# Optimization experiments

Measured on AMD Instinct MI355X. Metric: run time of the kernel, lower is better.

## Reference

```python
import jax, jax.numpy as jnp
import numpy as np

H = 1024      # hidden_size
V = 32000     # output_size (vocab)
L = 128       # max_length (encoder length)
B = 256       # batch


def setup_inputs() -> dict:
    key = jax.random.key(0)
    ks = jax.random.split(key, 16)
    s = 1.0 / np.sqrt(H)
    inp = {
        "input_ids": jax.random.randint(ks[0], (1, B), 0, V),
        "hidden": jax.random.normal(ks[1], (1, B, H), dtype=jnp.float32),
        "encoder_outputs": jax.random.normal(ks[2], (B, L, H), dtype=jnp.float32),
        # parameters
        "emb_table": jax.random.normal(ks[3], (V, H), dtype=jnp.float32),
        "attn_w": jax.random.uniform(ks[4], (L, 2 * H), jnp.float32, -s, s),
        "attn_b": jax.random.uniform(ks[5], (L,), jnp.float32, -s, s),
        "comb_w": jax.random.uniform(ks[6], (H, 2 * H), jnp.float32, -s, s),
        "comb_b": jax.random.uniform(ks[7], (H,), jnp.float32, -s, s),
        "w_ih": jax.random.uniform(ks[8], (3 * H, H), jnp.float32, -s, s),
        "b_ih": jax.random.uniform(ks[9], (3 * H,), jnp.float32, -s, s),
        "w_hh": jax.random.uniform(ks[10], (3 * H, H), jnp.float32, -s, s),
        "b_hh": jax.random.uniform(ks[11], (3 * H,), jnp.float32, -s, s),
        "out_w": jax.random.uniform(ks[12], (V, H), jnp.float32, -s, s),
        "out_b": jax.random.uniform(ks[13], (V,), jnp.float32, -s, s),
    }
    return inp


def reference(input_ids, hidden, encoder_outputs, emb_table,
              attn_w, attn_b, comb_w, comb_b,
              w_ih, b_ih, w_hh, b_hh, out_w, out_b):
    # embedding: input_ids (1, B) -> embedded (1, B, H); dropout is identity in eval
    embedded = emb_table[input_ids]            # (1, B, H)
    emb0 = embedded[0]                         # (B, H)
    h0 = hidden[0]                             # (B, H)

    # Bahdanau-style attention over fixed encoder length L
    attn_logits = jnp.concatenate([emb0, h0], axis=1) @ attn_w.T + attn_b   # (B, L)
    attn_weights = jax.nn.softmax(attn_logits, axis=1)                      # (B, L)
    attn_applied = jnp.einsum("bl,blh->bh", attn_weights, encoder_outputs)  # (B, H)

    # combine + relu
    x = jnp.concatenate([emb0, attn_applied], axis=1) @ comb_w.T + comb_b   # (B, H)
    x = jax.nn.relu(x)

    # single GRU step (PyTorch gate layout: r, z, n)
    gx = x @ w_ih.T + b_ih                     # (B, 3H)
    gh = h0 @ w_hh.T + b_hh                    # (B, 3H)
    xr, xz, xn = jnp.split(gx, 3, axis=1)
    hr, hz, hn = jnp.split(gh, 3, axis=1)
    r = jax.nn.sigmoid(xr + hr)
    z = jax.nn.sigmoid(xz + hz)
    n = jnp.tanh(xn + r * hn)
    h_new = (1.0 - z) * n + z * h0             # (B, H)

    logp = jax.nn.log_softmax(h_new @ out_w.T + out_b, axis=1)   # (B, V)
    return logp, h_new[None], attn_weights
```

## Files before the change

kernel.cpp:

```cpp
#include <hip/hip_runtime.h>
#include <hip/hip_bf16.h>
#include <math.h>

#define H 1024
#define L 128
#define B 256
#define V 32000

typedef __attribute__((ext_vector_type(8))) short bf16x8;
typedef __attribute__((ext_vector_type(4))) float f32x4;

static __device__ __forceinline__ ushort f2bf(float f) {
    unsigned int u = __float_as_uint(f);
    u += 0x7fffu + ((u >> 16) & 1u);
    return (ushort)(u >> 16);
}

__global__ __launch_bounds__(1024) void attn_kernel(
    const int* __restrict__ input_ids,
    const float* __restrict__ hidden,
    const float* __restrict__ enc,
    const float* __restrict__ emb_table,
    const float* __restrict__ attn_w,
    const float* __restrict__ attn_b,
    ushort* __restrict__ xcat_b16,
    ushort* __restrict__ h0_b16,
    float* __restrict__ attn_weights_out)
{
    __shared__ float s_e[H];
    __shared__ float s_h[H];
    __shared__ float s_w[L];
    __shared__ float s_r[4];
    __shared__ float4 s_pac[3 * 256];

    const int b = blockIdx.x;
    const int tid = threadIdx.x;

    if (tid < 256) {
        const int id = input_ids[b];
        float4 ev = ((const float4*)(emb_table + (size_t)id * H))[tid];
        ((float4*)s_e)[tid] = ev;
        uint2 p;
        p.x = (unsigned)f2bf(ev.x) | ((unsigned)f2bf(ev.y) << 16);
        p.y = (unsigned)f2bf(ev.z) | ((unsigned)f2bf(ev.w) << 16);
        *(uint2*)(xcat_b16 + (size_t)b * 2 * H + tid * 4) = p;
    } else if (tid < 512) {
        const int t = tid - 256;
        float4 hv = ((const float4*)(hidden + (size_t)b * H))[t];
        ((float4*)s_h)[t] = hv;
        uint2 q;
        q.x = (unsigned)f2bf(hv.x) | ((unsigned)f2bf(hv.y) << 16);
        q.y = (unsigned)f2bf(hv.z) | ((unsigned)f2bf(hv.w) << 16);
        *(uint2*)(h0_b16 + (size_t)b * H + t * 4) = q;
    }
    __syncthreads();

    {
        const int ll = tid >> 3;
        const int p = tid & 7;
        const float4* wv = (const float4*)(attn_w + (size_t)ll * (2 * H)) + p;
        const float4* se4 = (const float4*)s_e + p;
        const float4* sh4 = (const float4*)s_h + p;
        float acc = 0.f;
#pragma unroll 8
        for (int k = 0; k < 32; ++k) {
            float4 a = wv[k * 8];
            float4 s = se4[k * 8];
            acc += a.x * s.x + a.y * s.y + a.z * s.z + a.w * s.w;
        }
#pragma unroll 8
        for (int k = 0; k < 32; ++k) {
            float4 a = wv[256 + k * 8];
            float4 s = sh4[k * 8];
            acc += a.x * s.x + a.y * s.y + a.z * s.z + a.w * s.w;
        }
        acc += __shfl_xor(acc, 1);
        acc += __shfl_xor(acc, 2);
        acc += __shfl_xor(acc, 4);
        if (p == 0) s_w[ll] = acc + attn_b[ll];
    }
    __syncthreads();

    const int lane = tid & 63;
    if (tid < 128) {
        float v = s_w[tid];
        for (int off = 32; off; off >>= 1) v = fmaxf(v, __shfl_xor(v, off));
        if (lane == 0) s_r[tid >> 6] = v;
    }
    __syncthreads();
    if (tid < 128) {
        const float m = fmaxf(s_r[0], s_r[1]);
        float e = __expf(s_w[tid] - m);
        float sv = e;
        for (int off = 32; off; off >>= 1) sv += __shfl_xor(sv, off);
        if (lane == 0) s_r[2 + (tid >> 6)] = sv;
        s_w[tid] = e;
    }
    __syncthreads();
    if (tid < 128) {
        const float inv = 1.f / (s_r[2] + s_r[3]);
        const float wv = s_w[tid] * inv;
        s_w[tid] = wv;
        attn_weights_out[(size_t)b * L + tid] = wv;
    }
    __syncthreads();

    {
        const int grp = tid >> 8;
        const int c = tid & 255;
        const float4* enc4 = (const float4*)(enc + (size_t)b * L * H) + c;
        float ax = 0.f, ay = 0.f, az = 0.f, aw = 0.f;
#pragma unroll 8
        for (int q = 0; q < 32; ++q) {
            const int lidx = grp * 32 + q;
            const float wv = s_w[lidx];
            float4 ev = enc4[(size_t)lidx * 256];
            ax += wv * ev.x; ay += wv * ev.y; az += wv * ev.z; aw += wv * ev.w;
        }
        if (grp) {
            float4 t; t.x = ax; t.y = ay; t.z = az; t.w = aw;
            s_pac[(grp - 1) * 256 + c] = t;
        }
        __syncthreads();
        if (grp == 0) {
#pragma unroll
            for (int j = 0; j < 3; ++j) {
                float4 t = s_pac[j * 256 + c];
                ax += t.x; ay += t.y; az += t.z; aw += t.w;
            }
            uint2 p;
            p.x = (unsigned)f2bf(ax) | ((unsigned)f2bf(ay) << 16);
            p.y = (unsigned)f2bf(az) | ((unsigned)f2bf(aw) << 16);
            *(uint2*)(xcat_b16 + (size_t)b * 2 * H + H + c * 4) = p;
        }
    }
}

template<int K, int MT, int MODE>
__global__ __launch_bounds__(256, 2) void gemm_stream(
    const ushort* __restrict__ A,
    const float* __restrict__ W,
    const float* __restrict__ bias,
    float* __restrict__ outf,
    ushort* __restrict__ outb,
    float* __restrict__ rowsum,
    int N)
{
    constexpr int MFR = MT / 16;
    const int tid = threadIdx.x;
    const int wv = tid >> 6;
    const int l  = tid & 63;
    const int g  = l >> 4;
    const int ln = l & 15;

    const int row0 = blockIdx.x * MT;
    const int bn0  = blockIdx.y * 128 + wv * 32;

    const ushort* aptr = A + (size_t)(row0 + ln) * K + g * 8;
    const float*  wptr = W + (size_t)(bn0 + ln) * K + g * 8;

    f32x4 acc[MFR][2];
#pragma unroll
    for (int m = 0; m < MFR; ++m) {
        acc[m][0] = (f32x4){0.f, 0.f, 0.f, 0.f};
        acc[m][1] = (f32x4){0.f, 0.f, 0.f, 0.f};
    }

    bf16x8 aA[MFR][2], aB[MFR][2];
    float4 wA[2][2][2], wB[2][2][2];

    auto LOADM = [&](bf16x8 (&a)[MFR][2], float4 (&wf)[2][2][2], int k0) {
#pragma unroll
        for (int m = 0; m < MFR; ++m)
#pragma unroll
            for (int s = 0; s < 2; ++s)
                a[m][s] = *(const bf16x8*)(aptr + (size_t)16 * m * K + k0 + 32 * s);
#pragma unroll
        for (int n = 0; n < 2; ++n)
#pragma unroll
            for (int s = 0; s < 2; ++s) {
                const float* p = wptr + (size_t)16 * n * K + k0 + 32 * s;
                wf[n][s][0] = *(const float4*)p;
                wf[n][s][1] = *(const float4*)(p + 4);
            }
    };
    auto COMPUTE = [&](bf16x8 (&a)[MFR][2], float4 (&wf)[2][2][2]) {
#pragma unroll
        for (int s = 0; s < 2; ++s) {
            bf16x8 bw[2];
#pragma unroll
            for (int n = 0; n < 2; ++n) {
                ushort t[8];
                t[0] = f2bf(wf[n][s][0].x); t[1] = f2bf(wf[n][s][0].y);
                t[2] = f2bf(wf[n][s][0].z); t[3] = f2bf(wf[n][s][0].w);
                t[4] = f2bf(wf[n][s][1].x); t[5] = f2bf(wf[n][s][1].y);
                t[6] = f2bf(wf[n][s][1].z); t[7] = f2bf(wf[n][s][1].w);
                bw[n] = *(const bf16x8*)t;
            }
#pragma unroll
            for (int m = 0; m < MFR; ++m)
#pragma unroll
                for (int n = 0; n < 2; ++n)
                    acc[m][n] = __builtin_amdgcn_mfma_f32_16x16x32_bf16(
                        a[m][s], bw[n], acc[m][n], 0, 0, 0);
        }
    };

    LOADM(aA, wA, 0);
    for (int k0 = 0; k0 < K; k0 += 128) {
        LOADM(aB, wB, k0 + 64);
        COMPUTE(aA, wA);
        if (k0 + 128 < K) LOADM(aA, wA, k0 + 128);
        COMPUTE(aB, wB);
    }

    const float b0 = bias[bn0 + ln];
    const float b1 = bias[bn0 + 16 + ln];

    if (MODE == 0) {
#pragma unroll
        for (int m = 0; m < MFR; ++m)
#pragma unroll
            for (int n = 0; n < 2; ++n)
#pragma unroll
                for (int r = 0; r < 4; ++r)
                    outf[(size_t)(row0 + 16 * m + 4 * g + r) * N + bn0 + 16 * n + ln] =
                        acc[m][n][r] + (n ? b1 : b0);
    } else if (MODE == 1) {
#pragma unroll
        for (int m = 0; m < MFR; ++m)
#pragma unroll
            for (int n = 0; n < 2; ++n)
#pragma unroll
                for (int r = 0; r < 4; ++r) {
                    float vv = acc[m][n][r] + (n ? b1 : b0);
                    vv = fmaxf(vv, 0.f);
                    outb[(size_t)(row0 + 16 * m + 4 * g + r) * N + bn0 + 16 * n + ln] = f2bf(vv);
                }
    } else {
#pragma unroll
        for (int m = 0; m < MFR; ++m) {
            float e[4];
#pragma unroll
            for (int r = 0; r < 4; ++r) {
                const float v0 = acc[m][0][r] + b0;
                const float v1 = acc[m][1][r] + b1;
                const int row = row0 + 16 * m + 4 * g + r;
                outf[(size_t)row * N + bn0 + ln] = v0;
                outf[(size_t)row * N + bn0 + 16 + ln] = v1;
                e[r] = __expf(v0) + __expf(v1);
            }
#pragma unroll
            for (int msk = 1; msk < 16; msk <<= 1)
#pragma unroll
                for (int r = 0; r < 4; ++r)
                    e[r] += __shfl_xor(e[r], msk);
            if (ln < 4)
                atomicAdd(&rowsum[row0 + 16 * m + 4 * g + ln], e[ln]);
        }
    }
}

__global__ __launch_bounds__(256) void gru_kernel(
    const float* __restrict__ gx,
    const float* __restrict__ gh,
    const float* __restrict__ h0,
    float* __restrict__ h_new,
    ushort* __restrict__ hn_b16,
    float* __restrict__ rowsum)
{
    if (blockIdx.x == 0) rowsum[threadIdx.x] = 0.f;
    const int idx = blockIdx.x * 256 + threadIdx.x;
    const int b = idx >> 10;
    const int j = idx & (H - 1);
    const size_t base = (size_t)b * 3 * H;
    const float xr = gx[base + j];
    const float xz = gx[base + H + j];
    const float xn = gx[base + 2 * H + j];
    const float hr = gh[base + j];
    const float hz = gh[base + H + j];
    const float hn = gh[base + 2 * H + j];
    const float r = 1.f / (1.f + __expf(-(xr + hr)));
    const float z = 1.f / (1.f + __expf(-(xz + hz)));
    const float n = tanhf(xn + r * hn);
    const float out = (1.f - z) * n + z * h0[idx];
    h_new[idx] = out;
    hn_b16[idx] = f2bf(out);
}

__global__ __launch_bounds__(256) void logsm_kernel(
    float* __restrict__ logp,
    const float* __restrict__ rowsum)
{
    __shared__ float s_lse[B];
    if (threadIdx.x < B) s_lse[threadIdx.x] = __logf(rowsum[threadIdx.x]);
    __syncthreads();
    const int total4 = B * V / 4;
    for (int i = blockIdx.x * 256 + threadIdx.x; i < total4; i += gridDim.x * 256) {
        float4 v = ((const float4*)logp)[i];
        const int b = i / (V / 4);
        const float lse = s_lse[b];
        v.x -= lse; v.y -= lse; v.z -= lse; v.w -= lse;
        ((float4*)logp)[i] = v;
    }
}

extern "C" void kernel_launch(void* const* d_in, const int* in_sizes, int n_in,
                              void* d_out, int out_size, void* d_ws, size_t ws_size,
                              hipStream_t stream) {
    const int*   input_ids = (const int*)d_in[0];
    const float* hidden    = (const float*)d_in[1];
    const float* enc       = (const float*)d_in[2];
    const float* emb_table = (const float*)d_in[3];
    const float* attn_w    = (const float*)d_in[4];
    const float* attn_b    = (const float*)d_in[5];
    const float* comb_w    = (const float*)d_in[6];
    const float* comb_b    = (const float*)d_in[7];
    const float* w_ih      = (const float*)d_in[8];
    const float* b_ih      = (const float*)d_in[9];
    const float* w_hh      = (const float*)d_in[10];
    const float* b_hh      = (const float*)d_in[11];
    const float* out_w     = (const float*)d_in[12];
    const float* out_b     = (const float*)d_in[13];

    float* out = (float*)d_out;
    float* logp         = out;
    float* h_new        = out + (size_t)B * V;
    float* attn_weights = h_new + (size_t)B * H;

    ushort* xcat_b16 = (ushort*)d_ws;
    ushort* h0_b16   = xcat_b16 + (size_t)B * 2 * H;
    ushort* x_b16    = h0_b16 + (size_t)B * H;
    ushort* hn_b16   = x_b16 + (size_t)B * H;
    float*  gx       = (float*)(hn_b16 + (size_t)B * H);
    float*  gh       = gx + (size_t)B * 3 * H;
    float*  rowsum   = gh + (size_t)B * 3 * H;

    attn_kernel<<<dim3(B), dim3(1024), 0, stream>>>(
        input_ids, hidden, enc, emb_table, attn_w, attn_b,
        xcat_b16, h0_b16, attn_weights);

    gemm_stream<H, 16, 0><<<dim3(16, 24), dim3(256), 0, stream>>>(
        h0_b16, w_hh, b_hh, gh, nullptr, nullptr, 3 * H);

    gemm_stream<2 * H, 16, 1><<<dim3(16, 8), dim3(256), 0, stream>>>(
        xcat_b16, comb_w, comb_b, nullptr, x_b16, nullptr, H);

    gemm_stream<H, 16, 0><<<dim3(16, 24), dim3(256), 0, stream>>>(
        x_b16, w_ih, b_ih, gx, nullptr, nullptr, 3 * H);

    gru_kernel<<<dim3(B * H / 256), dim3(256), 0, stream>>>(
        gx, gh, hidden, h_new, hn_b16, rowsum);

    gemm_stream<H, 64, 4><<<dim3(4, 250), dim3(256), 0, stream>>>(
        hn_b16, out_w, out_b, logp, nullptr, rowsum, V);

    logsm_kernel<<<dim3(2048), dim3(256), 0, stream>>>(logp, rowsum);
}
```

Before: 591.0 us.

## Split attention kernel across two blocks per batch and retile GEMMs per column strip

The attention kernel now launches two blocks per batch row, each reducing half of the hidden columns of the encoder outputs, with 8 row groups instead of 4. The logits and softmax are recomputed in both blocks, and only the first one writes the shared outputs. The GEMMs change from (M-tile × 128-column) blocks to blocks that cover all 256 rows, where each of four waves handles 64 rows and each block handles a 32-column strip. This means every weight element is read by exactly one block, which removes the repeated weight streaming across M tiles. The cost is fewer, heavier blocks and duplicated attention-logit work.

After: 615.7 us. 4.2% more time.

```diff
diff --git a/kernel.cpp b/kernel.cpp
--- a/kernel.cpp
+++ b/kernel.cpp
@@ -16,7 +16,7 @@
     return (ushort)(u >> 16);
 }
 
-__global__ __launch_bounds__(1024) void attn_kernel(
+__global__ __launch_bounds__(1024, 8) void attn_kernel(
     const int* __restrict__ input_ids,
     const float* __restrict__ hidden,
     const float* __restrict__ enc,
@@ -31,27 +31,32 @@
     __shared__ float s_h[H];
     __shared__ float s_w[L];
     __shared__ float s_r[4];
-    __shared__ float4 s_pac[3 * 256];
+    __shared__ float4 s_pac[7 * 128];
 
     const int b = blockIdx.x;
+    const int hlf = blockIdx.y;
     const int tid = threadIdx.x;
 
     if (tid < 256) {
         const int id = input_ids[b];
         float4 ev = ((const float4*)(emb_table + (size_t)id * H))[tid];
         ((float4*)s_e)[tid] = ev;
-        uint2 p;
-        p.x = (unsigned)f2bf(ev.x) | ((unsigned)f2bf(ev.y) << 16);
-        p.y = (unsigned)f2bf(ev.z) | ((unsigned)f2bf(ev.w) << 16);
-        *(uint2*)(xcat_b16 + (size_t)b * 2 * H + tid * 4) = p;
+        if (hlf == 0) {
+            uint2 p;
+            p.x = (unsigned)f2bf(ev.x) | ((unsigned)f2bf(ev.y) << 16);
+            p.y = (unsigned)f2bf(ev.z) | ((unsigned)f2bf(ev.w) << 16);
+            *(uint2*)(xcat_b16 + (size_t)b * 2 * H + tid * 4) = p;
+        }
     } else if (tid < 512) {
         const int t = tid - 256;
         float4 hv = ((const float4*)(hidden + (size_t)b * H))[t];
         ((float4*)s_h)[t] = hv;
-        uint2 q;
-        q.x = (unsigned)f2bf(hv.x) | ((unsigned)f2bf(hv.y) << 16);
-        q.y = (unsigned)f2bf(hv.z) | ((unsigned)f2bf(hv.w) << 16);
-        *(uint2*)(h0_b16 + (size_t)b * H + t * 4) = q;
+        if (hlf == 0) {
+            uint2 q;
+            q.x = (unsigned)f2bf(hv.x) | ((unsigned)f2bf(hv.y) << 16);
+            q.y = (unsigned)f2bf(hv.z) | ((unsigned)f2bf(hv.w) << 16);
+            *(uint2*)(h0_b16 + (size_t)b * H + t * 4) = q;
+        }
     }
     __syncthreads();
 
@@ -62,13 +67,13 @@
         const float4* se4 = (const float4*)s_e + p;
         const float4* sh4 = (const float4*)s_h + p;
         float acc = 0.f;
-#pragma unroll 8
+#pragma unroll 4
         for (int k = 0; k < 32; ++k) {
             float4 a = wv[k * 8];
             float4 s = se4[k * 8];
             acc += a.x * s.x + a.y * s.y + a.z * s.z + a.w * s.w;
         }
-#pragma unroll 8
+#pragma unroll 4
         for (int k = 0; k < 32; ++k) {
             float4 a = wv[256 + k * 8];
             float4 s = sh4[k * 8];
@@ -101,42 +106,43 @@
         const float inv = 1.f / (s_r[2] + s_r[3]);
         const float wv = s_w[tid] * inv;
         s_w[tid] = wv;
-        attn_weights_out[(size_t)b * L + tid] = wv;
+        if (hlf == 0) attn_weights_out[(size_t)b * L + tid] = wv;
     }
     __syncthreads();
 
     {
-        const int grp = tid >> 8;
-        const int c = tid & 255;
-        const float4* enc4 = (const float4*)(enc + (size_t)b * L * H) + c;
+        const int grp = tid >> 7;
+        const int c = tid & 127;
+        const int col = hlf * 128 + c;
+        const float4* enc4 = (const float4*)(enc + (size_t)b * L * H) + col;
         float ax = 0.f, ay = 0.f, az = 0.f, aw = 0.f;
 #pragma unroll 8
-        for (int q = 0; q < 32; ++q) {
-            const int lidx = grp * 32 + q;
+        for (int q = 0; q < 16; ++q) {
+            const int lidx = grp * 16 + q;
             const float wv = s_w[lidx];
             float4 ev = enc4[(size_t)lidx * 256];
             ax += wv * ev.x; ay += wv * ev.y; az += wv * ev.z; aw += wv * ev.w;
         }
         if (grp) {
             float4 t; t.x = ax; t.y = ay; t.z = az; t.w = aw;
-            s_pac[(grp - 1) * 256 + c] = t;
+            s_pac[(grp - 1) * 128 + c] = t;
         }
         __syncthreads();
         if (grp == 0) {
 #pragma unroll
-            for (int j = 0; j < 3; ++j) {
-                float4 t = s_pac[j * 256 + c];
+            for (int j = 0; j < 7; ++j) {
+                float4 t = s_pac[j * 128 + c];
                 ax += t.x; ay += t.y; az += t.z; aw += t.w;
             }
             uint2 p;
             p.x = (unsigned)f2bf(ax) | ((unsigned)f2bf(ay) << 16);
             p.y = (unsigned)f2bf(az) | ((unsigned)f2bf(aw) << 16);
-            *(uint2*)(xcat_b16 + (size_t)b * 2 * H + H + c * 4) = p;
-        }
-    }
-}
-
-template<int K, int MT, int MODE>
+            *(uint2*)(xcat_b16 + (size_t)b * 2 * H + H + col * 4) = p;
+        }
+    }
+}
+
+template<int K, int MODE>
 __global__ __launch_bounds__(256, 2) void gemm_stream(
     const ushort* __restrict__ A,
     const float* __restrict__ W,
@@ -146,15 +152,15 @@
     float* __restrict__ rowsum,
     int N)
 {
-    constexpr int MFR = MT / 16;
+    constexpr int MFR = 4;
     const int tid = threadIdx.x;
     const int wv = tid >> 6;
     const int l  = tid & 63;
     const int g  = l >> 4;
     const int ln = l & 15;
 
-    const int row0 = blockIdx.x * MT;
-    const int bn0  = blockIdx.y * 128 + wv * 32;
+    const int row0 = wv * 64;
+    const int bn0  = blockIdx.x * 32;
 
     const ushort* aptr = A + (size_t)(row0 + ln) * K + g * 8;
     const float*  wptr = W + (size_t)(bn0 + ln) * K + g * 8;
@@ -336,23 +342,23 @@
     float*  gh       = gx + (size_t)B * 3 * H;
     float*  rowsum   = gh + (size_t)B * 3 * H;
 
-    attn_kernel<<<dim3(B), dim3(1024), 0, stream>>>(
+    attn_kernel<<<dim3(B, 2), dim3(1024), 0, stream>>>(
         input_ids, hidden, enc, emb_table, attn_w, attn_b,
         xcat_b16, h0_b16, attn_weights);
 
-    gemm_stream<H, 16, 0><<<dim3(16, 24), dim3(256), 0, stream>>>(
+    gemm_stream<H, 0><<<dim3(3 * H / 32), dim3(256), 0, stream>>>(
         h0_b16, w_hh, b_hh, gh, nullptr, nullptr, 3 * H);
 
-    gemm_stream<2 * H, 16, 1><<<dim3(16, 8), dim3(256), 0, stream>>>(
+    gemm_stream<2 * H, 1><<<dim3(H / 32), dim3(256), 0, stream>>>(
         xcat_b16, comb_w, comb_b, nullptr, x_b16, nullptr, H);
 
-    gemm_stream<H, 16, 0><<<dim3(16, 24), dim3(256), 0, stream>>>(
+    gemm_stream<H, 0><<<dim3(3 * H / 32), dim3(256), 0, stream>>>(
         x_b16, w_ih, b_ih, gx, nullptr, nullptr, 3 * H);
 
     gru_kernel<<<dim3(B * H / 256), dim3(256), 0, stream>>>(
         gx, gh, hidden, h_new, hn_b16, rowsum);
 
-    gemm_stream<H, 64, 4><<<dim3(4, 250), dim3(256), 0, stream>>>(
+    gemm_stream<H, 4><<<dim3(V / 32), dim3(256), 0, stream>>>(
         hn_b16, out_w, out_b, logp, nullptr, rowsum, V);
 
     logsm_kernel<<<dim3(2048), dim3(256), 0, stream>>>(logp, rowsum);
```
